# Performance work log

Hardware: AMD Instinct MI355X
Metric: run time of the kernel (lower is better)

## Reference

```python
import jax, jax.numpy as jnp
import numpy as np

B, H, V, A, NANN, DEPTH = 32, 256, 512, 3, 8, 7


def preorder_perm(arity, depth):
    # level-order node index -> pre-order position permutation for a full arity-ary tree
    starts = np.cumsum([0] + [arity ** l for l in range(depth + 1)])
    order = []
    def rec(l, p):
        order.append(int(starts[l] + p))
        if l < depth:
            for c in range(arity):
                rec(l + 1, p * arity + c)
    rec(0, 0)
    return np.asarray(order, dtype=np.int32)


def setup_inputs() -> dict:
    key = jax.random.key(0)
    ks = jax.random.split(key, 12)
    s = 0.05
    return {
        "root_hiddens": jax.random.normal(ks[0], (B, H), jnp.float32),
        "ann_table": jax.random.normal(ks[1], (NANN, H), jnp.float32),
        "w1": jax.random.normal(ks[2], (2 * H, H), jnp.float32) * s,
        "b1": jnp.zeros((2 * H,), jnp.float32),
        "w2": jax.random.normal(ks[3], (V, 2 * H), jnp.float32) * s,
        "b2": jnp.zeros((V,), jnp.float32),
        "gru_w_ih": jax.random.normal(ks[4], (A, 3 * H, H), jnp.float32) * s,
        "gru_w_hh": jax.random.normal(ks[5], (A, 3 * H, H), jnp.float32) * s,
        "gru_b_ih": jnp.zeros((A, 3 * H), jnp.float32),
        "gru_b_hh": jnp.zeros((A, 3 * H), jnp.float32),
        "ann_ids": jax.random.randint(ks[6], (B,), 0, NANN, jnp.int32),
        "depth": DEPTH,
    }


def _forward(root_hiddens, ann_table, w1, b1, w2, b2,
             gru_w_ih, gru_w_hh, gru_b_ih, gru_b_hh, ann_ids, depth):
    b, h = root_hiddens.shape
    arity = gru_w_ih.shape[0]
    x = ann_table[ann_ids]                                   # [B,H] annotation embedding (GRU input at every node)
    # input-side gates are constant across the whole tree: precompute once
    gx = jnp.einsum('bh,agh->bag', x, gru_w_ih) + gru_b_ih   # [B,A,3H]
    xr, xz, xn = jnp.split(gx, 3, axis=-1)                   # each [B,A,H]

    hid = root_hiddens[:, None, :]                           # [B,1,H]
    levels = [hid]
    for _ in range(depth):
        gh = jnp.einsum('bnh,agh->bnag', hid, gru_w_hh) + gru_b_hh  # [B,n,A,3H]
        hr, hz, hn = jnp.split(gh, 3, axis=-1)
        r = jax.nn.sigmoid(xr[:, None] + hr)
        z = jax.nn.sigmoid(xz[:, None] + hz)
        n = jnp.tanh(xn[:, None] + r * hn)
        new_h = (1.0 - z) * n + z * hid[:, :, None, :]       # [B,n,A,H]
        hid = new_h.reshape(b, -1, h)                        # child c of node p -> p*A+c
        levels.append(hid)

    all_h = jnp.concatenate(levels, axis=1)                  # [B,N,H] level-order
    mid = jax.nn.sigmoid(jnp.einsum('bnh,oh->bno', all_h, w1) + b1)
    prod = jnp.einsum('bno,vo->bnv', mid, w2) + b2           # [B,N,V]
    perm = jnp.asarray(preorder_perm(arity, depth))
    return jnp.transpose(prod[:, perm, :], (1, 0, 2))        # [N,B,V] (seq-first, like pad_sequence)


def reference(root_hiddens, ann_table, w1, b1, w2, b2,
              gru_w_ih, gru_w_hh, gru_b_ih, gru_b_hh, ann_ids, depth):
    return _forward(root_hiddens, ann_table, w1, b1, w2, b2,
                    gru_w_ih, gru_w_hh, gru_b_ih, gru_b_hh, ann_ids, depth)
```

## Files before the change

### kernel.cpp

```cpp
#include <hip/hip_runtime.h>
#include <hip/hip_bf16.h>
#include <stdint.h>
#include <stddef.h>

#define NB 32
#define NH 256
#define NMID 512
#define NV 512
#define NA 3
#define NDEPTH 7
#define NNODES 3280
#define NG 2304
#define MROWS (NNODES * NB)
#define HM 64

typedef __attribute__((ext_vector_type(8))) short bf16x8;
typedef __attribute__((ext_vector_type(4))) float f32x4;

__device__ __forceinline__ unsigned short f2bf(float x) {
    union { float f; unsigned u; } v; v.f = x;
    unsigned r = v.u + 0x7fffu + ((v.u >> 16) & 1u);
    return (unsigned short)(r >> 16);
}
__device__ __forceinline__ float bf2f(unsigned short u) {
    union { unsigned u; float f; } v; v.u = ((unsigned)u) << 16;
    return v.f;
}
__device__ __forceinline__ float sigm(float x) { return 1.0f / (1.0f + __expf(-x)); }
__device__ __forceinline__ float tanh_(float x) {
    x = fminf(fmaxf(x, -15.0f), 15.0f);
    float e = __expf(2.0f * x);
    return (e - 1.0f) / (e + 1.0f);
}
__device__ __forceinline__ f32x4 splat4(float s) { f32x4 v = {s, s, s, s}; return v; }

__global__ void cast_weights(const float* __restrict__ whh, const float* __restrict__ w1,
                             const float* __restrict__ w2,
                             unsigned short* __restrict__ whh_b,
                             unsigned short* __restrict__ w1_b,
                             unsigned short* __restrict__ w2_b) {
    const int n_whh = NG * NH;
    const int n_w1  = NMID * NH;
    const int n_w2  = NV * NMID;
    const int total = n_whh + n_w1 + n_w2;
    for (int i = blockIdx.x * blockDim.x + threadIdx.x; i < total;
         i += gridDim.x * blockDim.x) {
        if (i < n_whh) whh_b[i] = f2bf(whh[i]);
        else if (i < n_whh + n_w1) w1_b[i - n_whh] = f2bf(w1[i - n_whh]);
        else w2_b[i - n_whh - n_w1] = f2bf(w2[i - n_whh - n_w1]);
    }
}

__global__ void gx_kernel(const float* __restrict__ ann_table, const int* __restrict__ ann_ids,
                          const float* __restrict__ w_ih, const float* __restrict__ b_ih,
                          float* __restrict__ gx_t) {
    int gw = blockIdx.x * (blockDim.x >> 6) + (threadIdx.x >> 6);
    int lane = threadIdx.x & 63;
    if (gw >= NB * NG) return;
    int b = gw / NG;
    int col = gw - b * NG;
    const float* xr = ann_table + (size_t)ann_ids[b] * NH;
    const float* wr = w_ih + (size_t)col * NH;
    float4 xv = *(const float4*)(xr + lane * 4);
    float4 wv = *(const float4*)(wr + lane * 4);
    float s = xv.x * wv.x + xv.y * wv.y + xv.z * wv.z + xv.w * wv.w;
    #pragma unroll
    for (int off = 32; off; off >>= 1) s += __shfl_down(s, off);
    if (lane == 0) gx_t[(size_t)col * NB + b] = s + b_ih[col];
}

__global__ void init_root(const float* __restrict__ root, unsigned short* __restrict__ hid_b) {
    int i = blockIdx.x * blockDim.x + threadIdx.x;
    if (i < NB * NH) hid_b[i] = f2bf(root[i]);
}

__global__ void posmap_kernel(int* __restrict__ posmap) {
    int n = blockIdx.x * blockDim.x + threadIdx.x;
    if (n >= NNODES) return;
    int start = 0, cnt = 1, l = 0;
    while (n >= start + cnt) { start += cnt; cnt *= 3; l++; }
    int p = n - start;
    int pw = 1;
    for (int j = 0; j < l - 1; j++) pw *= 3;
    int pos = 0;
    for (int k = 1; k <= l; k++) {
        int d = (p / pw) % 3;
        int e = NDEPTH - k + 1;
        int p3 = 1; for (int j = 0; j < e; j++) p3 *= 3;
        pos += 1 + d * ((p3 - 1) / 2);
        pw /= 3;
    }
    posmap[n] = pos;
}

template<int NPB>
__global__ __launch_bounds__(512, 4)
void gru_level(const unsigned short* __restrict__ hid_b_in,
               unsigned short* __restrict__ hid_b_out,
               const unsigned short* __restrict__ whh_b,
               const float* __restrict__ b_hh, const float* __restrict__ gx_t,
               int start, int child_start, int cnt) {
    constexpr int M = 32 * NPB;
    __shared__ char a_s[M * 512];

    int tid = threadIdx.x;
    int lane = tid & 63;
    int wv = tid >> 6;
    int lr = lane & 15;
    int kg = (lane >> 4) * 8;
    int rbase = (lane >> 4) * 4;
    int nrel0 = blockIdx.x * NPB;
    size_t prow0 = (size_t)(start + nrel0) * NB;

    for (int c = tid; c < M * 32; c += 512) {
        int row = c >> 5;
        int coloff = (c & 31) * 8;
        bf16x8 v = *(const bf16x8*)(hid_b_in + (prow0 + row) * NH + coloff);
        *(bf16x8*)(a_s + ((row * 512 + coloff * 2) ^ ((row & 15) << 4))) = v;
    }
    __syncthreads();

    int Gb = (blockIdx.y * 8 + wv) * 16;
    int a = Gb >> 8;
    int colh = (Gb & 255) + lr;
    int gcol = a * 768 + colh;
    const unsigned short* bptr = whh_b + (size_t)(a * 512 + Gb + lr) * NH + kg;

    float bhr = b_hh[gcol], bhz = b_hh[gcol + 256], bhn = b_hh[gcol + 512];

    f32x4 acc[3][2 * NPB];
    #pragma unroll
    for (int g = 0; g < 2; ++g) {
        f32x4 gr = *(const f32x4*)(gx_t + (size_t)gcol * NB + g * 16 + rbase);
        f32x4 gz = *(const f32x4*)(gx_t + (size_t)(gcol + 256) * NB + g * 16 + rbase);
        #pragma unroll
        for (int mi = g; mi < 2 * NPB; mi += 2) {
            acc[0][mi] = gr + splat4(bhr);
            acc[1][mi] = gz + splat4(bhz);
            acc[2][mi] = splat4(bhn);
        }
    }

    bf16x8 bcur[3];
    #pragma unroll
    for (int t = 0; t < 3; ++t) bcur[t] = *(const bf16x8*)(bptr + t * 256 * NH);
    #pragma unroll
    for (int k0 = 0; k0 < NH; k0 += 32) {
        bf16x8 bnxt[3];
        if (k0 + 32 < NH) {
            #pragma unroll
            for (int t = 0; t < 3; ++t) bnxt[t] = *(const bf16x8*)(bptr + t * 256 * NH + k0 + 32);
        }
        bf16x8 af[2 * NPB];
        #pragma unroll
        for (int mi = 0; mi < 2 * NPB; ++mi) {
            int row = mi * 16 + lr;
            af[mi] = *(const bf16x8*)(a_s + ((row * 512 + (k0 + kg) * 2) ^ ((row & 15) << 4)));
        }
        #pragma unroll
        for (int t = 0; t < 3; ++t)
            #pragma unroll
            for (int mi = 0; mi < 2 * NPB; ++mi)
                acc[t][mi] = __builtin_amdgcn_mfma_f32_16x16x32_bf16(af[mi], bcur[t], acc[t][mi], 0, 0, 0);
        if (k0 + 32 < NH) {
            #pragma unroll
            for (int t = 0; t < 3; ++t) bcur[t] = bnxt[t];
        }
    }

    f32x4 gxn[2];
    #pragma unroll
    for (int g = 0; g < 2; ++g)
        gxn[g] = *(const f32x4*)(gx_t + (size_t)(gcol + 512) * NB + g * 16 + rbase);
    #pragma unroll
    for (int mi = 0; mi < 2 * NPB; ++mi) {
        #pragma unroll
        for (int j = 0; j < 4; ++j) {
            int row = mi * 16 + rbase + j;
            int ns = row >> 5;
            int b = row & 31;
            if (nrel0 + ns < cnt) {
                float r = sigm(acc[0][mi][j]);
                float z = sigm(acc[1][mi][j]);
                float nn = tanh_(gxn[mi & 1][j] + r * acc[2][mi][j]);
                unsigned short hpu = *(const unsigned short*)(a_s + ((row * 512 + colh * 2) ^ ((row & 15) << 4)));
                float hnew = (1.0f - z) * nn + z * bf2f(hpu);
                size_t crow = ((size_t)(child_start + (nrel0 + ns) * 3 + a)) * NB + b;
                hid_b_out[crow * NH + colh] = f2bf(hnew);
            }
        }
    }
}

__global__ __launch_bounds__(512, 4)
void head_fused(const unsigned short* __restrict__ hid_b,
                const unsigned short* __restrict__ w1_b, const float* __restrict__ b1,
                const unsigned short* __restrict__ w2_b, const float* __restrict__ b2,
                const int* __restrict__ posmap, float* __restrict__ out) {
    __shared__ char smem[HM * NMID * 2];

    int tid = threadIdx.x;
    int lane = tid & 63;
    int wv = tid >> 6;
    int mbase = blockIdx.x * HM;
    int lr = lane & 15;
    int kg = (lane >> 4) * 8;
    int rbase = (lane >> 4) * 4;
    int n0w = wv * 64;

    for (int c = tid; c < HM * 32; c += 512) {
        int row = c >> 5;
        int coloff = (c & 31) * 8;
        bf16x8 v = *(const bf16x8*)(hid_b + ((size_t)(mbase + row)) * NH + coloff);
        *(bf16x8*)(smem + ((row * 512 + coloff * 2) ^ ((row & 15) << 4))) = v;
    }
    __syncthreads();

    f32x4 acc[4][4];
    #pragma unroll
    for (int mi = 0; mi < 4; ++mi)
        #pragma unroll
        for (int ni = 0; ni < 4; ++ni) acc[mi][ni] = (f32x4){0.f, 0.f, 0.f, 0.f};

    {
        const unsigned short* bbase = w1_b + ((size_t)(n0w + lr)) * NH + kg;
        bf16x8 bcur[4];
        #pragma unroll
        for (int ni = 0; ni < 4; ++ni) bcur[ni] = *(const bf16x8*)(bbase + ni * 16 * NH);
        #pragma unroll
        for (int k0 = 0; k0 < NH; k0 += 32) {
            bf16x8 bnxt[4];
            if (k0 + 32 < NH) {
                #pragma unroll
                for (int ni = 0; ni < 4; ++ni) bnxt[ni] = *(const bf16x8*)(bbase + ni * 16 * NH + k0 + 32);
            }
            bf16x8 af[4];
            #pragma unroll
            for (int mi = 0; mi < 4; ++mi) {
                int row = mi * 16 + lr;
                af[mi] = *(const bf16x8*)(smem + ((row * 512 + (k0 + kg) * 2) ^ ((row & 15) << 4)));
            }
            #pragma unroll
            for (int mi = 0; mi < 4; ++mi)
                #pragma unroll
                for (int ni = 0; ni < 4; ++ni)
                    acc[mi][ni] = __builtin_amdgcn_mfma_f32_16x16x32_bf16(af[mi], bcur[ni], acc[mi][ni], 0, 0, 0);
            if (k0 + 32 < NH) {
                #pragma unroll
                for (int ni = 0; ni < 4; ++ni) bcur[ni] = bnxt[ni];
            }
        }
    }
    __syncthreads();

    #pragma unroll
    for (int mi = 0; mi < 4; ++mi)
        #pragma unroll
        for (int ni = 0; ni < 4; ++ni) {
            int col = n0w + ni * 16 + lr;
            float bv = b1[col];
            #pragma unroll
            for (int j = 0; j < 4; ++j) {
                int row = mi * 16 + rbase + j;
                float v = sigm(acc[mi][ni][j] + bv);
                *(unsigned short*)(smem + ((row * 1024 + col * 2) ^ ((row & 15) << 4))) = f2bf(v);
            }
        }
    __syncthreads();

    #pragma unroll
    for (int mi = 0; mi < 4; ++mi)
        #pragma unroll
        for (int ni = 0; ni < 4; ++ni) acc[mi][ni] = (f32x4){0.f, 0.f, 0.f, 0.f};
    {
        const unsigned short* bbase = w2_b + ((size_t)(n0w + lr)) * NMID + kg;
        bf16x8 bcur[4];
        #pragma unroll
        for (int ni = 0; ni < 4; ++ni) bcur[ni] = *(const bf16x8*)(bbase + ni * 16 * NMID);
        #pragma unroll
        for (int k0 = 0; k0 < NMID; k0 += 32) {
            bf16x8 bnxt[4];
            if (k0 + 32 < NMID) {
                #pragma unroll
                for (int ni = 0; ni < 4; ++ni) bnxt[ni] = *(const bf16x8*)(bbase + ni * 16 * NMID + k0 + 32);
            }
            bf16x8 af[4];
            #pragma unroll
            for (int mi = 0; mi < 4; ++mi) {
                int row = mi * 16 + lr;
                af[mi] = *(const bf16x8*)(smem + ((row * 1024 + (k0 + kg) * 2) ^ ((row & 15) << 4)));
            }
            #pragma unroll
            for (int mi = 0; mi < 4; ++mi)
                #pragma unroll
                for (int ni = 0; ni < 4; ++ni)
                    acc[mi][ni] = __builtin_amdgcn_mfma_f32_16x16x32_bf16(af[mi], bcur[ni], acc[mi][ni], 0, 0, 0);
            if (k0 + 32 < NMID) {
                #pragma unroll
                for (int ni = 0; ni < 4; ++ni) bcur[ni] = bnxt[ni];
            }
        }
    }
    #pragma unroll
    for (int mi = 0; mi < 4; ++mi)
        #pragma unroll
        for (int ni = 0; ni < 4; ++ni) {
            int col = n0w + ni * 16 + lr;
            float bv = b2[col];
            #pragma unroll
            for (int j = 0; j < 4; ++j) {
                int row = mbase + mi * 16 + rbase + j;
                int b = row & 31;
                int node = row >> 5;
                int pos = posmap[node];
                out[((size_t)pos * NB + b) * NV + col] = acc[mi][ni][j] + bv;
            }
        }
}

extern "C" void kernel_launch(void* const* d_in, const int* in_sizes, int n_in,
                              void* d_out, int out_size, void* d_ws, size_t ws_size,
                              hipStream_t stream) {
    const float* root      = (const float*)d_in[0];
    const float* ann_table = (const float*)d_in[1];
    const float* w1        = (const float*)d_in[2];
    const float* b1        = (const float*)d_in[3];
    const float* w2        = (const float*)d_in[4];
    const float* b2        = (const float*)d_in[5];
    const float* w_ih      = (const float*)d_in[6];
    const float* w_hh      = (const float*)d_in[7];
    const float* b_ih      = (const float*)d_in[8];
    const float* b_hh      = (const float*)d_in[9];
    const int*   ann_ids   = (const int*)d_in[10];

    uint8_t* ws = (uint8_t*)d_ws;
    unsigned short* whh_b = (unsigned short*)ws; ws += (size_t)NG * NH * 2;
    unsigned short* w1_b  = (unsigned short*)ws; ws += (size_t)NMID * NH * 2;
    unsigned short* w2_b  = (unsigned short*)ws; ws += (size_t)NV * NMID * 2;
    float* gx_t           = (float*)ws;          ws += (size_t)NB * NG * 4;
    int* posmap           = (int*)ws;            ws += (size_t)NNODES * 4;
    unsigned short* hid_b = (unsigned short*)ws; ws += (size_t)NNODES * NB * NH * 2;

    cast_weights<<<512, 256, 0, stream>>>(w_hh, w1, w2, whh_b, w1_b, w2_b);
    gx_kernel<<<(NB * NG) / 4, 256, 0, stream>>>(ann_table, ann_ids, w_ih, b_ih, gx_t);
    init_root<<<(NB * NH + 255) / 256, 256, 0, stream>>>(root, hid_b);
    posmap_kernel<<<(NNODES + 255) / 256, 256, 0, stream>>>(posmap);

    int start = 0, cnt = 1;
    for (int l = 0; l < NDEPTH; ++l) {
        int child_start = start + cnt;
        if (cnt >= 128) {
            gru_level<2><<<dim3((cnt + 1) / 2, 6), 512, 0, stream>>>(
                hid_b, hid_b, whh_b, b_hh, gx_t, start, child_start, cnt);
        } else {
            gru_level<1><<<dim3(cnt, 6), 512, 0, stream>>>(
                hid_b, hid_b, whh_b, b_hh, gx_t, start, child_start, cnt);
        }
        start = child_start; cnt *= 3;
    }
    head_fused<<<MROWS / HM, 512, 0, stream>>>(hid_b, w1_b, b1, w2_b, b2, posmap, (float*)d_out);
}
```

Before: 373.9 us.

## Use packed bf16 conversion, restructure epilogue stores, widen GRU tiles at deep levels

Replaces the software bf16 rounding with the hardware v_cvt_pk_bf16_f32 instruction in the GRU and head epilogues. It also hoists per-row index math and b2 loads out of inner loops in the head output store. For levels with 243 or more parent nodes the GRU kernel now processes 4 nodes per block instead of 2, with launch bounds relaxed to 2 waves/SIMD to allow more registers. Larger tiles raise register and LDS use and may reduce occupancy, and level 4 (81 nodes) now falls back to the NPB=1 path.

```diff
diff --git a/kernel.cpp b/kernel.cpp
--- a/kernel.cpp
+++ b/kernel.cpp
@@ -21,6 +21,11 @@
     union { float f; unsigned u; } v; v.f = x;
     unsigned r = v.u + 0x7fffu + ((v.u >> 16) & 1u);
     return (unsigned short)(r >> 16);
+}
+__device__ __forceinline__ unsigned cvt_pk_bf16(float a, float b) {
+    unsigned r;
+    asm("v_cvt_pk_bf16_f32 %0, %1, %2" : "=v"(r) : "v"(a), "v"(b));
+    return r;
 }
 __device__ __forceinline__ float bf2f(unsigned short u) {
     union { unsigned u; float f; } v; v.u = ((unsigned)u) << 16;
@@ -94,7 +99,7 @@
 }
 
 template<int NPB>
-__global__ __launch_bounds__(512, 4)
+__global__ __launch_bounds__(512, 2)
 void gru_level(const unsigned short* __restrict__ hid_b_in,
                unsigned short* __restrict__ hid_b_out,
                const unsigned short* __restrict__ whh_b,
@@ -174,21 +179,26 @@
         gxn[g] = *(const f32x4*)(gx_t + (size_t)(gcol + 512) * NB + g * 16 + rbase);
     #pragma unroll
     for (int mi = 0; mi < 2 * NPB; ++mi) {
+        int ns = (mi * 16 + rbase) >> 5;
+        if (nrel0 + ns >= cnt) continue;
+        size_t crow = ((size_t)(child_start + (nrel0 + ns) * 3 + a)) * NB;
+        float hnew[4];
         #pragma unroll
         for (int j = 0; j < 4; ++j) {
             int row = mi * 16 + rbase + j;
-            int ns = row >> 5;
-            int b = row & 31;
-            if (nrel0 + ns < cnt) {
-                float r = sigm(acc[0][mi][j]);
-                float z = sigm(acc[1][mi][j]);
-                float nn = tanh_(gxn[mi & 1][j] + r * acc[2][mi][j]);
-                unsigned short hpu = *(const unsigned short*)(a_s + ((row * 512 + colh * 2) ^ ((row & 15) << 4)));
-                float hnew = (1.0f - z) * nn + z * bf2f(hpu);
-                size_t crow = ((size_t)(child_start + (nrel0 + ns) * 3 + a)) * NB + b;
-                hid_b_out[crow * NH + colh] = f2bf(hnew);
-            }
-        }
+            float r = sigm(acc[0][mi][j]);
+            float z = sigm(acc[1][mi][j]);
+            float nn = tanh_(gxn[mi & 1][j] + r * acc[2][mi][j]);
+            unsigned short hpu = *(const unsigned short*)(a_s + ((row * 512 + colh * 2) ^ ((row & 15) << 4)));
+            hnew[j] = (1.0f - z) * nn + z * bf2f(hpu);
+        }
+        unsigned u01 = cvt_pk_bf16(hnew[0], hnew[1]);
+        unsigned u23 = cvt_pk_bf16(hnew[2], hnew[3]);
+        int b0 = (mi * 16 + rbase) & 31;
+        hid_b_out[(crow + b0 + 0) * NH + colh] = (unsigned short)u01;
+        hid_b_out[(crow + b0 + 1) * NH + colh] = (unsigned short)(u01 >> 16);
+        hid_b_out[(crow + b0 + 2) * NH + colh] = (unsigned short)u23;
+        hid_b_out[(crow + b0 + 3) * NH + colh] = (unsigned short)(u23 >> 16);
     }
 }
 
@@ -259,12 +269,17 @@
         for (int ni = 0; ni < 4; ++ni) {
             int col = n0w + ni * 16 + lr;
             float bv = b1[col];
-            #pragma unroll
-            for (int j = 0; j < 4; ++j) {
-                int row = mi * 16 + rbase + j;
-                float v = sigm(acc[mi][ni][j] + bv);
-                *(unsigned short*)(smem + ((row * 1024 + col * 2) ^ ((row & 15) << 4))) = f2bf(v);
-            }
+            float v0 = sigm(acc[mi][ni][0] + bv);
+            float v1 = sigm(acc[mi][ni][1] + bv);
+            float v2 = sigm(acc[mi][ni][2] + bv);
+            float v3 = sigm(acc[mi][ni][3] + bv);
+            unsigned u01 = cvt_pk_bf16(v0, v1);
+            unsigned u23 = cvt_pk_bf16(v2, v3);
+            int r0 = mi * 16 + rbase;
+            *(unsigned short*)(smem + (((r0 + 0) * 1024 + col * 2) ^ (((r0 + 0) & 15) << 4))) = (unsigned short)u01;
+            *(unsigned short*)(smem + (((r0 + 1) * 1024 + col * 2) ^ (((r0 + 1) & 15) << 4))) = (unsigned short)(u01 >> 16);
+            *(unsigned short*)(smem + (((r0 + 2) * 1024 + col * 2) ^ (((r0 + 2) & 15) << 4))) = (unsigned short)u23;
+            *(unsigned short*)(smem + (((r0 + 3) * 1024 + col * 2) ^ (((r0 + 3) & 15) << 4))) = (unsigned short)(u23 >> 16);
         }
     __syncthreads();
 
@@ -301,21 +316,23 @@
             }
         }
     }
-    #pragma unroll
-    for (int mi = 0; mi < 4; ++mi)
-        #pragma unroll
-        for (int ni = 0; ni < 4; ++ni) {
-            int col = n0w + ni * 16 + lr;
-            float bv = b2[col];
-            #pragma unroll
-            for (int j = 0; j < 4; ++j) {
-                int row = mbase + mi * 16 + rbase + j;
-                int b = row & 31;
-                int node = row >> 5;
-                int pos = posmap[node];
-                out[((size_t)pos * NB + b) * NV + col] = acc[mi][ni][j] + bv;
-            }
-        }
+    float bv4[4];
+    #pragma unroll
+    for (int ni = 0; ni < 4; ++ni) bv4[ni] = b2[n0w + ni * 16 + lr];
+    #pragma unroll
+    for (int mi = 0; mi < 4; ++mi) {
+        int row0 = mbase + mi * 16 + rbase;
+        #pragma unroll
+        for (int j = 0; j < 4; ++j) {
+            int row = row0 + j;
+            int b = row & 31;
+            int node = row >> 5;
+            float* orow = out + ((size_t)posmap[node] * NB + b) * NV + n0w + lr;
+            #pragma unroll
+            for (int ni = 0; ni < 4; ++ni)
+                orow[ni * 16] = acc[mi][ni][j] + bv4[ni];
+        }
+    }
 }
 
 extern "C" void kernel_launch(void* const* d_in, const int* in_sizes, int n_in,
@@ -349,8 +366,8 @@
     int start = 0, cnt = 1;
     for (int l = 0; l < NDEPTH; ++l) {
         int child_start = start + cnt;
-        if (cnt >= 128) {
-            gru_level<2><<<dim3((cnt + 1) / 2, 6), 512, 0, stream>>>(
+        if (cnt >= 243) {
+            gru_level<4><<<dim3((cnt + 3) / 4, 6), 512, 0, stream>>>(
                 hid_b, hid_b, whh_b, b_hh, gx_t, start, child_start, cnt);
         } else {
             gru_level<1><<<dim3(cnt, 6), 512, 0, stream>>>(
```

Result: no change. 380.9 us (+1.9%).
